# Performance work log

Hardware: AMD Instinct MI355X
Metric: run time of the kernel (lower is better)

The kernel has to match this reference:

```python
import jax, jax.numpy as jnp
import numpy as np

N, E, D, A, FC, B = 50000, 800000, 256, 7, 64, 512
EPS = 1e-5

def _glorot(key, fan_in, fan_out):
    lim = np.sqrt(6.0 / (fan_in + fan_out))
    return jax.random.uniform(key, (fan_in, fan_out), jnp.float32, -lim, lim)

def setup_inputs() -> dict:
    key = jax.random.key(0)
    ks = jax.random.split(key, 20)
    inp = {
        'x': jax.random.normal(ks[0], (N, 3), jnp.float32),
        'edge_index': jax.random.randint(ks[1], (2, E), 0, N, jnp.int32),
        'batch_index': jnp.sort(jax.random.randint(ks[2], (N,), 0, B, jnp.int32)),
        'a': jax.random.normal(ks[3], (B, A), jnp.float32),
        # GCNConv weights (lin weight + bias)
        'W0': _glorot(ks[4], 3, D),   'b0': jnp.zeros((D,), jnp.float32),
        'W1': _glorot(ks[5], D, D),   'b1': jnp.zeros((D,), jnp.float32),
        'W2': _glorot(ks[6], D, D),   'b2': jnp.zeros((D,), jnp.float32),
        'W3': _glorot(ks[7], D, D),   'b3': jnp.zeros((D,), jnp.float32),
        # action MLP
        'afc1_w': _glorot(ks[8], A, 8 * A),     'afc1_b': jnp.zeros((8 * A,), jnp.float32),
        'afc2_w': _glorot(ks[9], 8 * A, 8 * A), 'afc2_b': jnp.zeros((8 * A,), jnp.float32),
        'afc3_w': _glorot(ks[10], 8 * A, D),    'afc3_b': jnp.zeros((D,), jnp.float32),
        # head
        'fc1_w': _glorot(ks[11], D, FC), 'fc1_b': jnp.zeros((FC,), jnp.float32),
        'fc2_w': _glorot(ks[12], FC, 1), 'fc2_b': jnp.zeros((1,), jnp.float32),
        # LayerNorm affine params
        'ln1_g': jnp.ones((D,), jnp.float32),  'ln1_b': jnp.zeros((D,), jnp.float32),
        'ln2_g': jnp.ones((D,), jnp.float32),  'ln2_b': jnp.zeros((D,), jnp.float32),
        'ln4_g': jnp.ones((FC,), jnp.float32), 'ln4_b': jnp.zeros((FC,), jnp.float32),
        'ln5_g': jnp.ones((8 * A,), jnp.float32), 'ln5_b': jnp.zeros((8 * A,), jnp.float32),
    }
    return inp

def leaky(x):
    return jnp.where(x >= 0, x, 0.01 * x)

def layernorm(x, g, b):
    m = jnp.mean(x, axis=-1, keepdims=True)
    v = jnp.mean((x - m) ** 2, axis=-1, keepdims=True)
    return (x - m) * jax.lax.rsqrt(v + EPS) * g + b

def reference(x, edge_index, batch_index, a,
              W0, b0, W1, b1, W2, b2, W3, b3,
              afc1_w, afc1_b, afc2_w, afc2_b, afc3_w, afc3_b,
              fc1_w, fc1_b, fc2_w, fc2_b,
              ln1_g, ln1_b, ln2_g, ln2_b, ln4_g, ln4_b, ln5_g, ln5_b):
    n = x.shape[0]
    loop = jnp.arange(n, dtype=edge_index.dtype)
    src = jnp.concatenate([edge_index[0], loop])  # message sources
    dst = jnp.concatenate([edge_index[1], loop])  # message targets
    # symmetric GCN normalization with self-loops: deg over targets
    deg = jax.ops.segment_sum(jnp.ones_like(dst, dtype=x.dtype), dst, num_segments=n)
    dinv = jnp.where(deg > 0, jax.lax.rsqrt(deg), 0.0)
    norm = (dinv[src] * dinv[dst])[:, None]  # [E+N, 1]

    def gcn(h, W, bias):
        hw = h @ W
        agg = jax.ops.segment_sum(hw[src] * norm, dst, num_segments=n)
        return agg + bias

    h0 = gcn(x, W0, b0)
    h1 = leaky(gcn(h0, W1, b1)) + h0
    h2 = leaky(gcn(h1, W2, b2)) + h1
    h3 = leaky(gcn(h2, W3, b3)) + h2

    pooled = jax.ops.segment_max(h3, batch_index, num_segments=B)  # [B, D]
    V = layernorm(pooled, ln2_g, ln2_b)

    av = leaky(a @ afc1_w + afc1_b)
    av = layernorm(av, ln5_g, ln5_b)
    av = leaky(av @ afc2_w + afc2_b)
    av = leaky(av @ afc3_w + afc3_b)
    av = layernorm(av, ln1_g, ln1_b)

    z = V * av
    z = layernorm(leaky(z @ fc1_w + fc1_b), ln4_g, ln4_b)
    out = z @ fc2_w + fc2_b
    return out[:, 0]
```

## Files before the change

### kernel.cpp

```cpp
#include <hip/hip_runtime.h>

#define LN_EPS 1e-5f
#define SCAN_CHUNK 4096

typedef __bf16 bf16x8 __attribute__((ext_vector_type(8)));
typedef float f32x4 __attribute__((ext_vector_type(4)));

__device__ __forceinline__ float b2f(unsigned short s) {
    union { unsigned u; float f; } c; c.u = ((unsigned)s) << 16; return c.f;
}
__device__ __forceinline__ float blo(unsigned v) {
    union { unsigned u; float f; } c; c.u = v << 16; return c.f;
}
__device__ __forceinline__ float bhi(unsigned v) {
    union { unsigned u; float f; } c; c.u = v & 0xffff0000u; return c.f;
}
__device__ __forceinline__ unsigned short f2b(float f) {
    union { float f; unsigned u; } c; c.f = f;
    unsigned r = (c.u + 0x7FFFu + ((c.u >> 16) & 1u)) >> 16;
    return (unsigned short)r;
}
__device__ __forceinline__ float leaky(float x) { return x >= 0.f ? x : 0.01f * x; }


__global__ void init_kernel(int* ec, int* fill, int n) {
    int i = blockIdx.x * 256 + threadIdx.x;
    if (i < n) { ec[i] = 0; fill[i] = 0; }
}

__global__ void deg_kernel(const int* __restrict__ dst, int* ec, int e) {
    int i = blockIdx.x * 256 + threadIdx.x;
    if (i < e) atomicAdd(&ec[dst[i]], 1);
}

__global__ void scanA(const int* __restrict__ ec, int* __restrict__ bsum, int n) {
    __shared__ int red[4];
    int b = blockIdx.x, t = threadIdx.x;
    int base = b * SCAN_CHUNK + t * 16;
    int s = 0;
    #pragma unroll
    for (int k = 0; k < 16; ++k) { int i = base + k; if (i < n) s += ec[i]; }
    #pragma unroll
    for (int off = 32; off; off >>= 1) s += __shfl_down(s, off, 64);
    if ((t & 63) == 0) red[t >> 6] = s;
    __syncthreads();
    if (t == 0) bsum[b] = red[0] + red[1] + red[2] + red[3];
}

__global__ void scanB(int* bsum, int nb) {
    if (threadIdx.x == 0) {
        int acc = 0;
        for (int i = 0; i < nb; ++i) { int v = bsum[i]; bsum[i] = acc; acc += v; }
        bsum[nb] = acc;
    }
}

__global__ void scanC(const int* __restrict__ ec, const int* __restrict__ bsum,
                      int* __restrict__ ptr, int n, int nb) {
    __shared__ int wsum[4];
    int b = blockIdx.x, t = threadIdx.x, lane = t & 63, w = t >> 6;
    int base = b * SCAN_CHUNK + t * 16;
    int loc[16]; int s = 0;
    #pragma unroll
    for (int k = 0; k < 16; ++k) { int i = base + k; int v = (i < n) ? ec[i] : 0; loc[k] = s; s += v; }
    int x = s;
    #pragma unroll
    for (int off = 1; off < 64; off <<= 1) { int y = __shfl_up(x, off, 64); if (lane >= off) x += y; }
    if (lane == 63) wsum[w] = x;
    __syncthreads();
    int wexcl = 0;
    #pragma unroll
    for (int ww = 0; ww < 4; ++ww) if (ww < w) wexcl += wsum[ww];
    int toff = bsum[b] + wexcl + (x - s);
    #pragma unroll
    for (int k = 0; k < 16; ++k) { int i = base + k; if (i < n) ptr[i] = toff + loc[k]; }
    if (b == nb - 1 && t == 255) ptr[n] = bsum[nb];
}

__global__ void dinv_kernel(const int* __restrict__ ec, float* __restrict__ dinv, int n, int mpad) {
    int i = blockIdx.x * 256 + threadIdx.x;
    if (i < mpad) dinv[i] = (i < n) ? rsqrtf((float)(ec[i] + 1)) : 0.f;
}

__global__ void fill_kernel(const int* __restrict__ src, const int* __restrict__ dst,
                            const int* __restrict__ ptr, int* fill,
                            int* __restrict__ csrc, int e) {
    int i = blockIdx.x * 256 + threadIdx.x;
    if (i < e) {
        int d = dst[i];
        int pos = atomicAdd(&fill[d], 1);
        csrc[ptr[d] + pos] = src[i];
    }
}


__global__ void wt_kernel(const float* __restrict__ W1, const float* __restrict__ W2,
                          const float* __restrict__ W3, unsigned short* __restrict__ wt) {
    int k = blockIdx.x, l = blockIdx.y, nn = threadIdx.x;
    const float* W = (l == 0) ? W1 : (l == 1) ? W2 : W3;
    wt[l * 65536 + nn * 256 + k] = f2b(W[k * 256 + nn]);
}


__global__ void aggx_kernel(const float* __restrict__ x, const float* __restrict__ dinv,
                            const int* __restrict__ ptr, const int* __restrict__ csrc,
                            float* __restrict__ aggx, int n) {
    int i = blockIdx.x * 256 + threadIdx.x;
    if (i >= n) return;
    float di = dinv[i];
    float a0 = di * x[i * 3], a1 = di * x[i * 3 + 1], a2 = di * x[i * 3 + 2];
    float p0 = 0.f, p1 = 0.f, p2 = 0.f;
    float q0 = 0.f, q1 = 0.f, q2 = 0.f;
    float r0 = 0.f, r1 = 0.f, r2 = 0.f;
    int e0 = ptr[i], e1 = ptr[i + 1];
    int e = e0;
    for (; e + 4 <= e1; e += 4) {
        int s0 = csrc[e], s1 = csrc[e + 1], s2 = csrc[e + 2], s3 = csrc[e + 3];
        float d0 = dinv[s0], d1 = dinv[s1], d2 = dinv[s2], d3 = dinv[s3];
        a0 += d0 * x[s0 * 3]; a1 += d0 * x[s0 * 3 + 1]; a2 += d0 * x[s0 * 3 + 2];
        p0 += d1 * x[s1 * 3]; p1 += d1 * x[s1 * 3 + 1]; p2 += d1 * x[s1 * 3 + 2];
        q0 += d2 * x[s2 * 3]; q1 += d2 * x[s2 * 3 + 1]; q2 += d2 * x[s2 * 3 + 2];
        r0 += d3 * x[s3 * 3]; r1 += d3 * x[s3 * 3 + 1]; r2 += d3 * x[s3 * 3 + 2];
    }
    for (; e < e1; ++e) {
        int s = csrc[e]; float ds = dinv[s];
        a0 += ds * x[s * 3]; a1 += ds * x[s * 3 + 1]; a2 += ds * x[s * 3 + 2];
    }
    a0 += (p0 + q0) + r0; a1 += (p1 + q1) + r1; a2 += (p2 + q2) + r2;
    aggx[i * 3] = a0 * di; aggx[i * 3 + 1] = a1 * di; aggx[i * 3 + 2] = a2 * di;
}

__global__ __launch_bounds__(256) void h0_kernel(const float* __restrict__ aggx,
                          const float* __restrict__ W0, const float* __restrict__ b0,
                          const float* __restrict__ dinv,
                          float* __restrict__ h, unsigned short* __restrict__ hbs,
                          int n, int mpad) {
    int t = threadIdx.x;
    int row = blockIdx.x * 4 + (t >> 6);
    int f = (t & 63) * 4;
    if (row >= n) return;
    float a0 = aggx[row * 3], a1 = aggx[row * 3 + 1], a2 = aggx[row * 3 + 2];
    float4 w0 = *(const float4*)(W0 + f);
    float4 w1 = *(const float4*)(W0 + 256 + f);
    float4 w2 = *(const float4*)(W0 + 512 + f);
    float4 bb = *(const float4*)(b0 + f);
    float4 v;
    v.x = bb.x + a0 * w0.x + a1 * w1.x + a2 * w2.x;
    v.y = bb.y + a0 * w0.y + a1 * w1.y + a2 * w2.y;
    v.z = bb.z + a0 * w0.z + a1 * w1.z + a2 * w2.z;
    v.w = bb.w + a0 * w0.w + a1 * w1.w + a2 * w2.w;
    *(float4*)(h + (size_t)row * 256 + f) = v;
    float di = dinv[row];
    ushort4 o;
    o.x = f2b(di * v.x); o.y = f2b(di * v.y); o.z = f2b(di * v.z); o.w = f2b(di * v.w);
    *(ushort4*)(hbs + ((size_t)(f >> 5) * mpad + row) * 32 + (f & 31)) = o;
}


__global__ __launch_bounds__(256) void spmm_kernel(
    const unsigned short* __restrict__ hbs,
    const int* __restrict__ ptr, const int* __restrict__ csrc,
    const float* __restrict__ dinv,
    unsigned short* __restrict__ agg,
    int n, int mpad) {
    int chunk = blockIdx.x & 7;
    int g = blockIdx.x >> 3;
    int t = threadIdx.x;
    int node = g * 16 + (t >> 4);
    if (node >= n) return;
    int fl = t & 15;
    const char* cb = (const char*)(hbs + (size_t)chunk * mpad * 32);
    unsigned loff = (unsigned)(fl << 2);
    int e0 = ptr[node], e1 = ptr[node + 1];
    unsigned sv = *(const unsigned*)(cb + (((unsigned)node << 6) | loff));
    float a0 = blo(sv), a1 = bhi(sv);
    float p0 = 0.f, p1 = 0.f, q0 = 0.f, q1 = 0.f, r0 = 0.f, r1 = 0.f, s0 = 0.f, s1 = 0.f;
    int len = e1 - e0;
    int nblk = (len + 7) >> 3;
    int e1m = e1 - 1;
    int idx[8];
    if (nblk > 0) {
        #pragma unroll
        for (int j = 0; j < 8; ++j) idx[j] = csrc[min(e0 + j, e1m)];
    }
    int e = e0;
    for (int b = 0; b < nblk; ++b) {
        int nidx[8];
        bool more = (b + 1 < nblk);
        int en = e + 8;
        #pragma unroll
        for (int j = 0; j < 8; ++j) if (more) nidx[j] = csrc[min(en + j, e1m)];
        unsigned u[8];
        #pragma unroll
        for (int j = 0; j < 8; ++j) u[j] = *(const unsigned*)(cb + (((unsigned)idx[j] << 6) | loff));
        #pragma unroll
        for (int j = 0; j < 8; ++j) if (e + j >= e1) u[j] = 0u;
        a0 += blo(u[0]); a1 += bhi(u[0]);
        p0 += blo(u[1]); p1 += bhi(u[1]);
        q0 += blo(u[2]); q1 += bhi(u[2]);
        r0 += blo(u[3]); r1 += bhi(u[3]);
        s0 += blo(u[4]); s1 += bhi(u[4]);
        a0 += blo(u[5]); a1 += bhi(u[5]);
        p0 += blo(u[6]); p1 += bhi(u[6]);
        q0 += blo(u[7]); q1 += bhi(u[7]);
        #pragma unroll
        for (int j = 0; j < 8; ++j) idx[j] = nidx[j];
        e = en;
    }
    a0 += (p0 + q0) + (r0 + s0);
    a1 += (p1 + q1) + (r1 + s1);
    float di = dinv[node];
    unsigned ob = ((unsigned)f2b(di * a1) << 16) | (unsigned)f2b(di * a0);
    *(unsigned*)((char*)agg + (size_t)chunk * mpad * 64 + (((unsigned)node << 6) | loff)) = ob;
}


__global__ __launch_bounds__(256) void gemm_kernel(const unsigned short* __restrict__ A,
                                                   const unsigned short* __restrict__ Bt,
                                                   const float* __restrict__ bias,
                                                   const float* __restrict__ dinv,
                                                   float* __restrict__ h,
                                                   unsigned short* __restrict__ hbs,
                                                   int mpad, int write_hbs) {
    const int K = 256;
    int wid = threadIdx.x >> 6, lane = threadIdx.x & 63;
    int m0 = blockIdx.x * 64;
    int n0 = wid * 64;
    int lr = lane & 15, lg = lane >> 4;
    f32x4 acc[4][4];
    #pragma unroll
    for (int i = 0; i < 4; i++)
        #pragma unroll
        for (int j = 0; j < 4; j++) acc[i][j] = (f32x4)(0.f);
    const unsigned short* Ap = A + ((size_t)(m0 + lr)) * 32 + lg * 8;
    const unsigned short* Bp = Bt + (size_t)(n0 + lr) * K + lg * 8;
    #pragma unroll
    for (int kc = 0; kc < 8; ++kc) {
        bf16x8 af[4], bfr[4];
        #pragma unroll
        for (int mi = 0; mi < 4; mi++)
            af[mi] = *(const bf16x8*)(Ap + (size_t)kc * mpad * 32 + mi * 512);
        #pragma unroll
        for (int ni = 0; ni < 4; ni++)
            bfr[ni] = *(const bf16x8*)(Bp + (size_t)ni * 16 * K + kc * 32);
        #pragma unroll
        for (int mi = 0; mi < 4; mi++)
            #pragma unroll
            for (int ni = 0; ni < 4; ni++)
                acc[mi][ni] = __builtin_amdgcn_mfma_f32_16x16x32_bf16(af[mi], bfr[ni], acc[mi][ni], 0, 0, 0);
    }
    #pragma unroll
    for (int mi = 0; mi < 4; mi++) {
        int r0 = m0 + mi * 16 + lg * 4;
        float4 dv = *(const float4*)(dinv + r0);
        #pragma unroll
        for (int ni = 0; ni < 4; ni++) {
            int c = n0 + ni * 16 + lr;
            float bv = bias[c];
            int ch = c >> 5, cf = c & 31;
            float vr[4];
            #pragma unroll
            for (int j = 0; j < 4; ++j) {
                size_t ho = (size_t)(r0 + j) * 256 + c;
                float v = leaky(acc[mi][ni][j] + bv) + h[ho];
                h[ho] = v;
                vr[j] = v;
            }
            if (write_hbs) {
                unsigned short* hp = hbs + ((size_t)ch * mpad + r0) * 32 + cf;
                hp[0]  = f2b(vr[0] * dv.x);
                hp[32] = f2b(vr[1] * dv.y);
                hp[64] = f2b(vr[2] * dv.z);
                hp[96] = f2b(vr[3] * dv.w);
            }
        }
    }
}


__global__ __launch_bounds__(256) void pool_kernel(const float* __restrict__ h,
                                                   const int* __restrict__ batch,
                                                   float* __restrict__ pooled, int n) {
    int b = blockIdx.x, d = threadIdx.x;
    int lo = 0, hi = n;
    while (lo < hi) { int m = (lo + hi) >> 1; if (batch[m] < b) lo = m + 1; else hi = m; }
    int s = lo;
    lo = 0; hi = n;
    while (lo < hi) { int m = (lo + hi) >> 1; if (batch[m] < b + 1) lo = m + 1; else hi = m; }
    int e = lo;
    float mx = -3.402823466e38f;
    for (int r = s; r < e; ++r) mx = fmaxf(mx, h[(size_t)r * 256 + d]);
    pooled[(size_t)b * 256 + d] = mx;
}


__device__ __forceinline__ float blk_sum(float v, float* red) {
    #pragma unroll
    for (int off = 32; off; off >>= 1) v += __shfl_down(v, off, 64);
    int lane = threadIdx.x & 63, wid = threadIdx.x >> 6;
    if (lane == 0) red[wid] = v;
    __syncthreads();
    float s = red[0] + red[1] + red[2] + red[3];
    __syncthreads();
    return s;
}

__global__ __launch_bounds__(256) void head_kernel(
    const float* __restrict__ pooled, const float* __restrict__ a,
    const float* __restrict__ afc1_w, const float* __restrict__ afc1_b,
    const float* __restrict__ afc2_w, const float* __restrict__ afc2_b,
    const float* __restrict__ afc3_w, const float* __restrict__ afc3_b,
    const float* __restrict__ fc1_w, const float* __restrict__ fc1_b,
    const float* __restrict__ fc2_w, const float* __restrict__ fc2_b,
    const float* __restrict__ ln1_g, const float* __restrict__ ln1_b,
    const float* __restrict__ ln2_g, const float* __restrict__ ln2_b,
    const float* __restrict__ ln4_g, const float* __restrict__ ln4_b,
    const float* __restrict__ ln5_g, const float* __restrict__ ln5_b,
    float* __restrict__ out) {
    __shared__ float red[4];
    __shared__ float sM[2];
    __shared__ float s1[56], s2[56], sZ[256], sT[64];
    int b = blockIdx.x, tid = threadIdx.x;

    float pv = pooled[(size_t)b * 256 + tid];
    float m = blk_sum(pv, red) * (1.f / 256.f);
    float d0 = pv - m;
    float var = blk_sum(d0 * d0, red) * (1.f / 256.f);
    float V = d0 * rsqrtf(var + LN_EPS) * ln2_g[tid] + ln2_b[tid];

    if (tid < 56) {
        float acc = afc1_b[tid];
        #pragma unroll
        for (int k = 0; k < 7; ++k) acc += a[b * 7 + k] * afc1_w[k * 56 + tid];
        s1[tid] = leaky(acc);
    }
    __syncthreads();
    if (tid == 0) {
        float s = 0.f; for (int k = 0; k < 56; ++k) s += s1[k];
        float mm = s / 56.f;
        float q = 0.f; for (int k = 0; k < 56; ++k) { float d = s1[k] - mm; q += d * d; }
        sM[0] = mm; sM[1] = rsqrtf(q / 56.f + LN_EPS);
    }
    __syncthreads();
    if (tid < 56) s1[tid] = (s1[tid] - sM[0]) * sM[1] * ln5_g[tid] + ln5_b[tid];
    __syncthreads();
    if (tid < 56) {
        float acc = afc2_b[tid];
        for (int k = 0; k < 56; ++k) acc += s1[k] * afc2_w[k * 56 + tid];
        s2[tid] = leaky(acc);
    }
    __syncthreads();
    float acc = afc3_b[tid];
    for (int k = 0; k < 56; ++k) acc += s2[k] * afc3_w[k * 256 + tid];
    acc = leaky(acc);
    m = blk_sum(acc, red) * (1.f / 256.f);
    d0 = acc - m;
    var = blk_sum(d0 * d0, red) * (1.f / 256.f);
    float av = d0 * rsqrtf(var + LN_EPS) * ln1_g[tid] + ln1_b[tid];

    float z = V * av;
    sZ[tid] = z;
    __syncthreads();
    if (tid < 64) {
        float a2 = fc1_b[tid];
        for (int k = 0; k < 256; ++k) a2 += sZ[k] * fc1_w[k * 64 + tid];
        sT[tid] = leaky(a2);
    }
    __syncthreads();
    if (tid == 0) {
        float s = 0.f; for (int k = 0; k < 64; ++k) s += sT[k];
        float mm = s / 64.f;
        float q = 0.f; for (int k = 0; k < 64; ++k) { float d = sT[k] - mm; q += d * d; }
        float r = rsqrtf(q / 64.f + LN_EPS);
        float o = fc2_b[0];
        for (int k = 0; k < 64; ++k) {
            float zz = (sT[k] - mm) * r * ln4_g[k] + ln4_b[k];
            o += zz * fc2_w[k];
        }
        out[b] = o;
    }
}


extern "C" void kernel_launch(void* const* d_in, const int* in_sizes, int n_in,
                              void* d_out, int out_size, void* d_ws, size_t ws_size,
                              hipStream_t stream) {
    const float* x     = (const float*)d_in[0];
    const int*   eidx  = (const int*)d_in[1];
    const int*   batch = (const int*)d_in[2];
    const float* a     = (const float*)d_in[3];
    const float* W0 = (const float*)d_in[4];  const float* b0 = (const float*)d_in[5];
    const float* W1 = (const float*)d_in[6];  const float* b1 = (const float*)d_in[7];
    const float* W2 = (const float*)d_in[8];  const float* b2 = (const float*)d_in[9];
    const float* W3 = (const float*)d_in[10]; const float* b3 = (const float*)d_in[11];
    const float* afc1_w = (const float*)d_in[12]; const float* afc1_b = (const float*)d_in[13];
    const float* afc2_w = (const float*)d_in[14]; const float* afc2_b = (const float*)d_in[15];
    const float* afc3_w = (const float*)d_in[16]; const float* afc3_b = (const float*)d_in[17];
    const float* fc1_w  = (const float*)d_in[18]; const float* fc1_b  = (const float*)d_in[19];
    const float* fc2_w  = (const float*)d_in[20]; const float* fc2_b  = (const float*)d_in[21];
    const float* ln1_g = (const float*)d_in[22]; const float* ln1_b = (const float*)d_in[23];
    const float* ln2_g = (const float*)d_in[24]; const float* ln2_b = (const float*)d_in[25];
    const float* ln4_g = (const float*)d_in[26]; const float* ln4_b = (const float*)d_in[27];
    const float* ln5_g = (const float*)d_in[28]; const float* ln5_b = (const float*)d_in[29];

    int N = in_sizes[0] / 3;
    int E = in_sizes[1] / 2;
    int B = in_sizes[3] / 7;
    int Mpad = ((N + 63) / 64) * 64;
    int NB = (N + SCAN_CHUNK - 1) / SCAN_CHUNK;

    char* p = (char*)d_ws;
    auto alloc = [&](size_t bytes) -> char* {
        char* r = p; p += (bytes + 255) & ~(size_t)255; return r;
    };
    int*   ec   = (int*)alloc((size_t)N * 4);
    int*   fill = (int*)alloc((size_t)N * 4);
    int*   ptr  = (int*)alloc((size_t)(N + 1) * 4);
    int*   bsum = (int*)alloc((size_t)(NB + 1) * 4);
    int*   csrc = (int*)alloc((size_t)E * 4);
    float* dinv = (float*)alloc((size_t)Mpad * 4);
    float* aggx = (float*)alloc((size_t)N * 3 * 4);
    float* h    = (float*)alloc((size_t)Mpad * 256 * 4);
    unsigned short* hbs = (unsigned short*)alloc((size_t)Mpad * 256 * 2);
    unsigned short* agg = (unsigned short*)alloc((size_t)Mpad * 256 * 2);
    unsigned short* wt  = (unsigned short*)alloc((size_t)3 * 65536 * 2);
    float* pooled = (float*)alloc((size_t)B * 256 * 4);

    const int* srcl = eidx;
    const int* dstl = eidx + E;

    init_kernel<<<(N + 255) / 256, 256, 0, stream>>>(ec, fill, N);
    deg_kernel<<<(E + 255) / 256, 256, 0, stream>>>(dstl, ec, E);
    scanA<<<NB, 256, 0, stream>>>(ec, bsum, N);
    scanB<<<1, 64, 0, stream>>>(bsum, NB);
    scanC<<<NB, 256, 0, stream>>>(ec, bsum, ptr, N, NB);
    dinv_kernel<<<(Mpad + 255) / 256, 256, 0, stream>>>(ec, dinv, N, Mpad);
    fill_kernel<<<(E + 255) / 256, 256, 0, stream>>>(srcl, dstl, ptr, fill, csrc, E);
    wt_kernel<<<dim3(256, 3), 256, 0, stream>>>(W1, W2, W3, wt);
    aggx_kernel<<<(N + 255) / 256, 256, 0, stream>>>(x, dinv, ptr, csrc, aggx, N);
    h0_kernel<<<(N + 3) / 4, 256, 0, stream>>>(aggx, W0, b0, dinv, h, hbs, N, Mpad);

    const float* biases[3] = { b1, b2, b3 };
    int ngrp = (N + 15) / 16;
    for (int l = 0; l < 3; ++l) {
        spmm_kernel<<<ngrp * 8, 256, 0, stream>>>(hbs, ptr, csrc, dinv, agg, N, Mpad);
        gemm_kernel<<<Mpad / 64, 256, 0, stream>>>(agg, wt + (size_t)l * 65536, biases[l],
                                                   dinv, h, hbs, Mpad, (l < 2) ? 1 : 0);
    }

    pool_kernel<<<B, 256, 0, stream>>>(h, batch, pooled, N);
    head_kernel<<<B, 256, 0, stream>>>(pooled, a,
        afc1_w, afc1_b, afc2_w, afc2_b, afc3_w, afc3_b,
        fc1_w, fc1_b, fc2_w, fc2_b,
        ln1_g, ln1_b, ln2_g, ln2_b, ln4_g, ln4_b, ln5_g, ln5_b,
        (float*)d_out);
}
```

Measured before the change: 614.2 us.

## Pad CSR rows to 8, pre-shift indices, widen SpMM loads, fuse pooling into GEMM

```diff
diff --git a/kernel.cpp b/kernel.cpp
--- a/kernel.cpp
+++ b/kernel.cpp
@@ -5,22 +5,34 @@
 
 typedef __bf16 bf16x8 __attribute__((ext_vector_type(8)));
 typedef float f32x4 __attribute__((ext_vector_type(4)));
+typedef float f32x2 __attribute__((ext_vector_type(2)));
 
 __device__ __forceinline__ float b2f(unsigned short s) {
     union { unsigned u; float f; } c; c.u = ((unsigned)s) << 16; return c.f;
-}
-__device__ __forceinline__ float blo(unsigned v) {
-    union { unsigned u; float f; } c; c.u = v << 16; return c.f;
-}
-__device__ __forceinline__ float bhi(unsigned v) {
-    union { unsigned u; float f; } c; c.u = v & 0xffff0000u; return c.f;
 }
 __device__ __forceinline__ unsigned short f2b(float f) {
     union { float f; unsigned u; } c; c.f = f;
     unsigned r = (c.u + 0x7FFFu + ((c.u >> 16) & 1u)) >> 16;
     return (unsigned short)r;
 }
+__device__ __forceinline__ f32x2 up2(unsigned u) {
+    union { unsigned u; float f; } lo, hi;
+    lo.u = u << 16; hi.u = u & 0xffff0000u;
+    f32x2 r; r.x = lo.f; r.y = hi.f; return r;
+}
+__device__ __forceinline__ unsigned pk2(f32x2 v) {
+    return ((unsigned)f2b(v.y) << 16) | (unsigned)f2b(v.x);
+}
 __device__ __forceinline__ float leaky(float x) { return x >= 0.f ? x : 0.01f * x; }
+__device__ __forceinline__ unsigned encf(float f) {
+    union { float f; unsigned u; } c; c.f = f;
+    return ((int)c.u < 0) ? ~c.u : (c.u | 0x80000000u);
+}
+__device__ __forceinline__ float decf(unsigned u) {
+    union { unsigned u; float f; } c;
+    c.u = (u & 0x80000000u) ? (u & 0x7FFFFFFFu) : ~u;
+    return c.f;
+}
 
 
 __global__ void init_kernel(int* ec, int* fill, int n) {
@@ -39,7 +51,7 @@
     int base = b * SCAN_CHUNK + t * 16;
     int s = 0;
     #pragma unroll
-    for (int k = 0; k < 16; ++k) { int i = base + k; if (i < n) s += ec[i]; }
+    for (int k = 0; k < 16; ++k) { int i = base + k; if (i < n) s += (ec[i] + 7) & ~7; }
     #pragma unroll
     for (int off = 32; off; off >>= 1) s += __shfl_down(s, off, 64);
     if ((t & 63) == 0) red[t >> 6] = s;
@@ -62,7 +74,10 @@
     int base = b * SCAN_CHUNK + t * 16;
     int loc[16]; int s = 0;
     #pragma unroll
-    for (int k = 0; k < 16; ++k) { int i = base + k; int v = (i < n) ? ec[i] : 0; loc[k] = s; s += v; }
+    for (int k = 0; k < 16; ++k) {
+        int i = base + k; int v = (i < n) ? ((ec[i] + 7) & ~7) : 0;
+        loc[k] = s; s += v;
+    }
     int x = s;
     #pragma unroll
     for (int off = 1; off < 64; off <<= 1) { int y = __shfl_up(x, off, 64); if (lane >= off) x += y; }
@@ -80,6 +95,23 @@
 __global__ void dinv_kernel(const int* __restrict__ ec, float* __restrict__ dinv, int n, int mpad) {
     int i = blockIdx.x * 256 + threadIdx.x;
     if (i < mpad) dinv[i] = (i < n) ? rsqrtf((float)(ec[i] + 1)) : 0.f;
+}
+
+__global__ void xp_kernel(const float* __restrict__ x, const float* __restrict__ dinv,
+                          float4* __restrict__ xp, int n, int mpad) {
+    int i = blockIdx.x * 256 + threadIdx.x;
+    if (i >= mpad) return;
+    float4 v = make_float4(0.f, 0.f, 0.f, 0.f);
+    if (i < n) {
+        float d = dinv[i];
+        v.x = d * x[i * 3]; v.y = d * x[i * 3 + 1]; v.z = d * x[i * 3 + 2];
+    }
+    xp[i] = v;
+}
+
+__global__ void csrc_init_kernel(const int* __restrict__ ptr, int* __restrict__ csrc, int n) {
+    int i = blockIdx.x * 256 + threadIdx.x;
+    if (i < ptr[n]) csrc[i] = n << 6;
 }
 
 __global__ void fill_kernel(const int* __restrict__ src, const int* __restrict__ dst,
@@ -89,7 +121,7 @@
     if (i < e) {
         int d = dst[i];
         int pos = atomicAdd(&fill[d], 1);
-        csrc[ptr[d] + pos] = src[i];
+        csrc[ptr[d] + pos] = src[i] << 6;
     }
 }
 
@@ -102,31 +134,31 @@
 }
 
 
-__global__ void aggx_kernel(const float* __restrict__ x, const float* __restrict__ dinv,
+__global__ void aggx_kernel(const float4* __restrict__ xp, const float* __restrict__ dinv,
                             const int* __restrict__ ptr, const int* __restrict__ csrc,
                             float* __restrict__ aggx, int n) {
     int i = blockIdx.x * 256 + threadIdx.x;
     if (i >= n) return;
-    float di = dinv[i];
-    float a0 = di * x[i * 3], a1 = di * x[i * 3 + 1], a2 = di * x[i * 3 + 2];
+    const char* xb = (const char*)xp;
+    float4 self = xp[i];
+    float a0 = self.x, a1 = self.y, a2 = self.z;
     float p0 = 0.f, p1 = 0.f, p2 = 0.f;
     float q0 = 0.f, q1 = 0.f, q2 = 0.f;
     float r0 = 0.f, r1 = 0.f, r2 = 0.f;
     int e0 = ptr[i], e1 = ptr[i + 1];
-    int e = e0;
-    for (; e + 4 <= e1; e += 4) {
-        int s0 = csrc[e], s1 = csrc[e + 1], s2 = csrc[e + 2], s3 = csrc[e + 3];
-        float d0 = dinv[s0], d1 = dinv[s1], d2 = dinv[s2], d3 = dinv[s3];
-        a0 += d0 * x[s0 * 3]; a1 += d0 * x[s0 * 3 + 1]; a2 += d0 * x[s0 * 3 + 2];
-        p0 += d1 * x[s1 * 3]; p1 += d1 * x[s1 * 3 + 1]; p2 += d1 * x[s1 * 3 + 2];
-        q0 += d2 * x[s2 * 3]; q1 += d2 * x[s2 * 3 + 1]; q2 += d2 * x[s2 * 3 + 2];
-        r0 += d3 * x[s3 * 3]; r1 += d3 * x[s3 * 3 + 1]; r2 += d3 * x[s3 * 3 + 2];
-    }
-    for (; e < e1; ++e) {
-        int s = csrc[e]; float ds = dinv[s];
-        a0 += ds * x[s * 3]; a1 += ds * x[s * 3 + 1]; a2 += ds * x[s * 3 + 2];
+    for (int e = e0; e < e1; e += 4) {
+        int4 v = *(const int4*)(csrc + e);
+        float4 u0 = *(const float4*)(xb + (((unsigned)v.x) >> 2));
+        float4 u1 = *(const float4*)(xb + (((unsigned)v.y) >> 2));
+        float4 u2 = *(const float4*)(xb + (((unsigned)v.z) >> 2));
+        float4 u3 = *(const float4*)(xb + (((unsigned)v.w) >> 2));
+        a0 += u0.x; a1 += u0.y; a2 += u0.z;
+        p0 += u1.x; p1 += u1.y; p2 += u1.z;
+        q0 += u2.x; q1 += u2.y; q2 += u2.z;
+        r0 += u3.x; r1 += u3.y; r2 += u3.z;
     }
     a0 += (p0 + q0) + r0; a1 += (p1 + q1) + r1; a2 += (p2 + q2) + r2;
+    float di = dinv[i];
     aggx[i * 3] = a0 * di; aggx[i * 3 + 1] = a1 * di; aggx[i * 3 + 2] = a2 * di;
 }
 
@@ -138,22 +170,28 @@
     int t = threadIdx.x;
     int row = blockIdx.x * 4 + (t >> 6);
     int f = (t & 63) * 4;
-    if (row >= n) return;
-    float a0 = aggx[row * 3], a1 = aggx[row * 3 + 1], a2 = aggx[row * 3 + 2];
-    float4 w0 = *(const float4*)(W0 + f);
-    float4 w1 = *(const float4*)(W0 + 256 + f);
-    float4 w2 = *(const float4*)(W0 + 512 + f);
-    float4 bb = *(const float4*)(b0 + f);
-    float4 v;
-    v.x = bb.x + a0 * w0.x + a1 * w1.x + a2 * w2.x;
-    v.y = bb.y + a0 * w0.y + a1 * w1.y + a2 * w2.y;
-    v.z = bb.z + a0 * w0.z + a1 * w1.z + a2 * w2.z;
-    v.w = bb.w + a0 * w0.w + a1 * w1.w + a2 * w2.w;
-    *(float4*)(h + (size_t)row * 256 + f) = v;
-    float di = dinv[row];
-    ushort4 o;
-    o.x = f2b(di * v.x); o.y = f2b(di * v.y); o.z = f2b(di * v.z); o.w = f2b(di * v.w);
-    *(ushort4*)(hbs + ((size_t)(f >> 5) * mpad + row) * 32 + (f & 31)) = o;
+    if (row >= mpad) return;
+    unsigned short* hp = hbs + ((size_t)(f >> 5) * mpad + row) * 32 + (f & 31);
+    if (row < n) {
+        float a0 = aggx[row * 3], a1 = aggx[row * 3 + 1], a2 = aggx[row * 3 + 2];
+        float4 w0 = *(const float4*)(W0 + f);
+        float4 w1 = *(const float4*)(W0 + 256 + f);
+        float4 w2 = *(const float4*)(W0 + 512 + f);
+        float4 bb = *(const float4*)(b0 + f);
+        float4 v;
+        v.x = bb.x + a0 * w0.x + a1 * w1.x + a2 * w2.x;
+        v.y = bb.y + a0 * w0.y + a1 * w1.y + a2 * w2.y;
+        v.z = bb.z + a0 * w0.z + a1 * w1.z + a2 * w2.z;
+        v.w = bb.w + a0 * w0.w + a1 * w1.w + a2 * w2.w;
+        *(float4*)(h + (size_t)row * 256 + f) = v;
+        float di = dinv[row];
+        ushort4 o;
+        o.x = f2b(di * v.x); o.y = f2b(di * v.y); o.z = f2b(di * v.z); o.w = f2b(di * v.w);
+        *(ushort4*)hp = o;
+    } else {
+        ushort4 o; o.x = 0; o.y = 0; o.z = 0; o.w = 0;
+        *(ushort4*)hp = o;
+    }
 }
 
 
@@ -166,52 +204,48 @@
     int chunk = blockIdx.x & 7;
     int g = blockIdx.x >> 3;
     int t = threadIdx.x;
-    int node = g * 16 + (t >> 4);
+    int node = g * 64 + (t >> 2);
     if (node >= n) return;
-    int fl = t & 15;
-    const char* cb = (const char*)(hbs + (size_t)chunk * mpad * 32);
-    unsigned loff = (unsigned)(fl << 2);
+    unsigned loff = (unsigned)((t & 3) << 4);
+    const char* cb = (const char*)hbs + (size_t)chunk * mpad * 64;
     int e0 = ptr[node], e1 = ptr[node + 1];
-    unsigned sv = *(const unsigned*)(cb + (((unsigned)node << 6) | loff));
-    float a0 = blo(sv), a1 = bhi(sv);
-    float p0 = 0.f, p1 = 0.f, q0 = 0.f, q1 = 0.f, r0 = 0.f, r1 = 0.f, s0 = 0.f, s1 = 0.f;
-    int len = e1 - e0;
-    int nblk = (len + 7) >> 3;
-    int e1m = e1 - 1;
-    int idx[8];
-    if (nblk > 0) {
-        #pragma unroll
-        for (int j = 0; j < 8; ++j) idx[j] = csrc[min(e0 + j, e1m)];
-    }
+    uint4 own = *(const uint4*)(cb + (((unsigned)node << 6) | loff));
+    f32x2 accA0 = up2(own.x), accA1 = up2(own.y), accA2 = up2(own.z), accA3 = up2(own.w);
+    f32x2 accB0 = (f32x2)(0.f), accB1 = (f32x2)(0.f), accB2 = (f32x2)(0.f), accB3 = (f32x2)(0.f);
     int e = e0;
-    for (int b = 0; b < nblk; ++b) {
-        int nidx[8];
-        bool more = (b + 1 < nblk);
+    int4 ia, ib;
+    if (e < e1) { ia = *(const int4*)(csrc + e); ib = *(const int4*)(csrc + e + 4); }
+    while (e < e1) {
         int en = e + 8;
-        #pragma unroll
-        for (int j = 0; j < 8; ++j) if (more) nidx[j] = csrc[min(en + j, e1m)];
-        unsigned u[8];
-        #pragma unroll
-        for (int j = 0; j < 8; ++j) u[j] = *(const unsigned*)(cb + (((unsigned)idx[j] << 6) | loff));
-        #pragma unroll
-        for (int j = 0; j < 8; ++j) if (e + j >= e1) u[j] = 0u;
-        a0 += blo(u[0]); a1 += bhi(u[0]);
-        p0 += blo(u[1]); p1 += bhi(u[1]);
-        q0 += blo(u[2]); q1 += bhi(u[2]);
-        r0 += blo(u[3]); r1 += bhi(u[3]);
-        s0 += blo(u[4]); s1 += bhi(u[4]);
-        a0 += blo(u[5]); a1 += bhi(u[5]);
-        p0 += blo(u[6]); p1 += bhi(u[6]);
-        q0 += blo(u[7]); q1 += bhi(u[7]);
-        #pragma unroll
-        for (int j = 0; j < 8; ++j) idx[j] = nidx[j];
-        e = en;
-    }
-    a0 += (p0 + q0) + (r0 + s0);
-    a1 += (p1 + q1) + (r1 + s1);
+        int4 na, nb;
+        if (en < e1) { na = *(const int4*)(csrc + en); nb = *(const int4*)(csrc + en + 4); }
+        uint4 u0 = *(const uint4*)(cb + ((unsigned)ia.x | loff));
+        uint4 u1 = *(const uint4*)(cb + ((unsigned)ia.y | loff));
+        uint4 u2 = *(const uint4*)(cb + ((unsigned)ia.z | loff));
+        uint4 u3 = *(const uint4*)(cb + ((unsigned)ia.w | loff));
+        uint4 u4 = *(const uint4*)(cb + ((unsigned)ib.x | loff));
+        uint4 u5 = *(const uint4*)(cb + ((unsigned)ib.y | loff));
+        uint4 u6 = *(const uint4*)(cb + ((unsigned)ib.z | loff));
+        uint4 u7 = *(const uint4*)(cb + ((unsigned)ib.w | loff));
+        accA0 += up2(u0.x); accA1 += up2(u0.y); accA2 += up2(u0.z); accA3 += up2(u0.w);
+        accB0 += up2(u1.x); accB1 += up2(u1.y); accB2 += up2(u1.z); accB3 += up2(u1.w);
+        accA0 += up2(u2.x); accA1 += up2(u2.y); accA2 += up2(u2.z); accA3 += up2(u2.w);
+        accB0 += up2(u3.x); accB1 += up2(u3.y); accB2 += up2(u3.z); accB3 += up2(u3.w);
+        accA0 += up2(u4.x); accA1 += up2(u4.y); accA2 += up2(u4.z); accA3 += up2(u4.w);
+        accB0 += up2(u5.x); accB1 += up2(u5.y); accB2 += up2(u5.z); accB3 += up2(u5.w);
+        accA0 += up2(u6.x); accA1 += up2(u6.y); accA2 += up2(u6.z); accA3 += up2(u6.w);
+        accB0 += up2(u7.x); accB1 += up2(u7.y); accB2 += up2(u7.z); accB3 += up2(u7.w);
+        ia = na; ib = nb; e = en;
+    }
     float di = dinv[node];
-    unsigned ob = ((unsigned)f2b(di * a1) << 16) | (unsigned)f2b(di * a0);
-    *(unsigned*)((char*)agg + (size_t)chunk * mpad * 64 + (((unsigned)node << 6) | loff)) = ob;
+    f32x2 dd; dd.x = di; dd.y = di;
+    accA0 = (accA0 + accB0) * dd;
+    accA1 = (accA1 + accB1) * dd;
+    accA2 = (accA2 + accB2) * dd;
+    accA3 = (accA3 + accB3) * dd;
+    uint4 o;
+    o.x = pk2(accA0); o.y = pk2(accA1); o.z = pk2(accA2); o.w = pk2(accA3);
+    *(uint4*)((char*)agg + (size_t)chunk * mpad * 64 + (((unsigned)node << 6) | loff)) = o;
 }
 
 
@@ -221,10 +255,18 @@
                                                    const float* __restrict__ dinv,
                                                    float* __restrict__ h,
                                                    unsigned short* __restrict__ hbs,
-                                                   int mpad, int write_hbs) {
+                                                   const int* __restrict__ batch,
+                                                   unsigned* __restrict__ pooledu,
+                                                   int mpad, int n, int write_hbs, int last) {
     const int K = 256;
+    __shared__ int sb[64];
     int wid = threadIdx.x >> 6, lane = threadIdx.x & 63;
     int m0 = blockIdx.x * 64;
+    if (last && threadIdx.x < 64) {
+        int r = m0 + threadIdx.x;
+        sb[threadIdx.x] = (r < n) ? batch[r] : -1;
+    }
+    __syncthreads();
     int n0 = wid * 64;
     int lr = lane & 15, lg = lane >> 4;
     f32x4 acc[4][4];
@@ -249,48 +291,63 @@
             for (int ni = 0; ni < 4; ni++)
                 acc[mi][ni] = __builtin_amdgcn_mfma_f32_16x16x32_bf16(af[mi], bfr[ni], acc[mi][ni], 0, 0, 0);
     }
-    #pragma unroll
-    for (int mi = 0; mi < 4; mi++) {
-        int r0 = m0 + mi * 16 + lg * 4;
-        float4 dv = *(const float4*)(dinv + r0);
+    if (!last) {
+        #pragma unroll
+        for (int mi = 0; mi < 4; mi++) {
+            int r0 = m0 + mi * 16 + lg * 4;
+            float4 dv = *(const float4*)(dinv + r0);
+            #pragma unroll
+            for (int ni = 0; ni < 4; ni++) {
+                int c = n0 + ni * 16 + lr;
+                float bv = bias[c];
+                int ch = c >> 5, cf = c & 31;
+                float vr[4];
+                #pragma unroll
+                for (int j = 0; j < 4; ++j) {
+                    size_t ho = (size_t)(r0 + j) * 256 + c;
+                    float v = leaky(acc[mi][ni][j] + bv) + h[ho];
+                    h[ho] = v;
+                    vr[j] = v;
+                }
+                if (write_hbs) {
+                    unsigned short* hp = hbs + ((size_t)ch * mpad + r0) * 32 + cf;
+                    hp[0]  = f2b(vr[0] * dv.x);
+                    hp[32] = f2b(vr[1] * dv.y);
+                    hp[64] = f2b(vr[2] * dv.z);
+                    hp[96] = f2b(vr[3] * dv.w);
+                }
+            }
+        }
+    } else {
         #pragma unroll
         for (int ni = 0; ni < 4; ni++) {
             int c = n0 + ni * 16 + lr;
             float bv = bias[c];
-            int ch = c >> 5, cf = c & 31;
-            float vr[4];
+            int cs = -1; float cm = 0.f;
             #pragma unroll
-            for (int j = 0; j < 4; ++j) {
-                size_t ho = (size_t)(r0 + j) * 256 + c;
-                float v = leaky(acc[mi][ni][j] + bv) + h[ho];
-                h[ho] = v;
-                vr[j] = v;
+            for (int mi = 0; mi < 4; mi++) {
+                int rb = mi * 16 + lg * 4;
+                #pragma unroll
+                for (int j = 0; j < 4; ++j) {
+                    int seg = sb[rb + j];
+                    float v = leaky(acc[mi][ni][j] + bv) + h[(size_t)(m0 + rb + j) * 256 + c];
+                    if (seg >= 0) {
+                        if (seg != cs) {
+                            if (cs >= 0) atomicMax(pooledu + (size_t)cs * 256 + c, encf(cm));
+                            cs = seg; cm = v;
+                        } else {
+                            cm = fmaxf(cm, v);
+                        }
+                    }
+                }
             }
-            if (write_hbs) {
-                unsigned short* hp = hbs + ((size_t)ch * mpad + r0) * 32 + cf;
-                hp[0]  = f2b(vr[0] * dv.x);
-                hp[32] = f2b(vr[1] * dv.y);
-                hp[64] = f2b(vr[2] * dv.z);
-                hp[96] = f2b(vr[3] * dv.w);
-            }
+            if (cs >= 0) atomicMax(pooledu + (size_t)cs * 256 + c, encf(cm));
         }
     }
 }
 
-
-__global__ __launch_bounds__(256) void pool_kernel(const float* __restrict__ h,
-                                                   const int* __restrict__ batch,
-                                                   float* __restrict__ pooled, int n) {
-    int b = blockIdx.x, d = threadIdx.x;
-    int lo = 0, hi = n;
-    while (lo < hi) { int m = (lo + hi) >> 1; if (batch[m] < b) lo = m + 1; else hi = m; }
-    int s = lo;
-    lo = 0; hi = n;
-    while (lo < hi) { int m = (lo + hi) >> 1; if (batch[m] < b + 1) lo = m + 1; else hi = m; }
-    int e = lo;
-    float mx = -3.402823466e38f;
-    for (int r = s; r < e; ++r) mx = fmaxf(mx, h[(size_t)r * 256 + d]);
-    pooled[(size_t)b * 256 + d] = mx;
+__global__ void pool_init_kernel(unsigned* pooledu) {
+    pooledu[blockIdx.x * 256 + threadIdx.x] = 0u;
 }
 
 
@@ -306,7 +363,7 @@
 }
 
 __global__ __launch_bounds__(256) void head_kernel(
-    const float* __restrict__ pooled, const float* __restrict__ a,
+    const unsigned* __restrict__ pooledu, const float* __restrict__ a,
     const float* __restrict__ afc1_w, const float* __restrict__ afc1_b,
     const float* __restrict__ afc2_w, const float* __restrict__ afc2_b,
     const float* __restrict__ afc3_w, const float* __restrict__ afc3_b,
@@ -322,7 +379,7 @@
     __shared__ float s1[56], s2[56], sZ[256], sT[64];
     int b = blockIdx.x, tid = threadIdx.x;
 
-    float pv = pooled[(size_t)b * 256 + tid];
+    float pv = decf(pooledu[(size_t)b * 256 + tid]);
     float m = blk_sum(pv, red) * (1.f / 256.f);
     float d0 = pv - m;
     float var = blk_sum(d0 * d0, red) * (1.f / 256.f);
@@ -408,6 +465,7 @@
     int B = in_sizes[3] / 7;
     int Mpad = ((N + 63) / 64) * 64;
     int NB = (N + SCAN_CHUNK - 1) / SCAN_CHUNK;
+    int Ecap = E + 7 * N + 8;
 
     char* p = (char*)d_ws;
     auto alloc = [&](size_t bytes) -> char* {
@@ -417,14 +475,15 @@
     int*   fill = (int*)alloc((size_t)N * 4);
     int*   ptr  = (int*)alloc((size_t)(N + 1) * 4);
     int*   bsum = (int*)alloc((size_t)(NB + 1) * 4);
-    int*   csrc = (int*)alloc((size_t)E * 4);
+    int*   csrc = (int*)alloc((size_t)Ecap * 4);
     float* dinv = (float*)alloc((size_t)Mpad * 4);
+    float4* xp  = (float4*)alloc((size_t)Mpad * 16);
     float* aggx = (float*)alloc((size_t)N * 3 * 4);
     float* h    = (float*)alloc((size_t)Mpad * 256 * 4);
     unsigned short* hbs = (unsigned short*)alloc((size_t)Mpad * 256 * 2);
     unsigned short* agg = (unsigned short*)alloc((size_t)Mpad * 256 * 2);
     unsigned short* wt  = (unsigned short*)alloc((size_t)3 * 65536 * 2);
-    float* pooled = (float*)alloc((size_t)B * 256 * 4);
+    unsigned* pooledu = (unsigned*)alloc((size_t)B * 256 * 4);
 
     const int* srcl = eidx;
     const int* dstl = eidx + E;
@@ -435,21 +494,24 @@
     scanB<<<1, 64, 0, stream>>>(bsum, NB);
     scanC<<<NB, 256, 0, stream>>>(ec, bsum, ptr, N, NB);
     dinv_kernel<<<(Mpad + 255) / 256, 256, 0, stream>>>(ec, dinv, N, Mpad);
+    xp_kernel<<<(Mpad + 255) / 256, 256, 0, stream>>>(x, dinv, xp, N, Mpad);
+    csrc_init_kernel<<<(Ecap + 255) / 256, 256, 0, stream>>>(ptr, csrc, N);
     fill_kernel<<<(E + 255) / 256, 256, 0, stream>>>(srcl, dstl, ptr, fill, csrc, E);
     wt_kernel<<<dim3(256, 3), 256, 0, stream>>>(W1, W2, W3, wt);
-    aggx_kernel<<<(N + 255) / 256, 256, 0, stream>>>(x, dinv, ptr, csrc, aggx, N);
-    h0_kernel<<<(N + 3) / 4, 256, 0, stream>>>(aggx, W0, b0, dinv, h, hbs, N, Mpad);
+    aggx_kernel<<<(N + 255) / 256, 256, 0, stream>>>(xp, dinv, ptr, csrc, aggx, N);
+    h0_kernel<<<Mpad / 4, 256, 0, stream>>>(aggx, W0, b0, dinv, h, hbs, N, Mpad);
+    pool_init_kernel<<<B, 256, 0, stream>>>(pooledu);
 
     const float* biases[3] = { b1, b2, b3 };
-    int ngrp = (N + 15) / 16;
+    int nblkN = (N + 63) / 64;
     for (int l = 0; l < 3; ++l) {
-        spmm_kernel<<<ngrp * 8, 256, 0, stream>>>(hbs, ptr, csrc, dinv, agg, N, Mpad);
+        spmm_kernel<<<nblkN * 8, 256, 0, stream>>>(hbs, ptr, csrc, dinv, agg, N, Mpad);
         gemm_kernel<<<Mpad / 64, 256, 0, stream>>>(agg, wt + (size_t)l * 65536, biases[l],
-                                                   dinv, h, hbs, Mpad, (l < 2) ? 1 : 0);
-    }
-
-    pool_kernel<<<B, 256, 0, stream>>>(h, batch, pooled, N);
-    head_kernel<<<B, 256, 0, stream>>>(pooled, a,
+                                                   dinv, h, hbs, batch, pooledu,
+                                                   Mpad, N, (l < 2) ? 1 : 0, (l == 2) ? 1 : 0);
+    }
+
+    head_kernel<<<B, 256, 0, stream>>>(pooledu, a,
         afc1_w, afc1_b, afc2_w, afc2_b, afc3_w, afc3_b,
         fc1_w, fc1_b, fc2_w, fc2_b,
         ln1_g, ln1_b, ln2_g, ln2_b, ln4_g, ln4_b, ln5_g, ln5_b,
```

After: 561.3 us. -8.6%, faster.
